# Optimization experiments

Hardware: AMD Instinct MI355X
Metric: run time of the kernel (lower is better)

The kernel has to match this reference:

```python
import jax, jax.numpy as jnp
import numpy as np

N_HEAD = 16    # config.n_head
T_STEPS = 3    # config.T: PC energy-minimization steps
LR = 0.01      # config.local_learning_rate


def _causal_attention(x, Wq, Wk, Wv):
    # x: [B, S, E] latent activity; generative model f(x) = causal MHA(x)
    B, S, E = x.shape
    D = E // N_HEAD
    def split(h):  # [B,S,E] -> [B,H,S,D]
        return h.reshape(B, S, N_HEAD, D).transpose(0, 2, 1, 3)
    q = split(x @ Wq.T)
    k = split(x @ Wk.T)
    v = split(x @ Wv.T)
    scores = jnp.einsum('bhqd,bhkd->bhqk', q, k) / jnp.sqrt(jnp.asarray(D, x.dtype))
    mask = jnp.tril(jnp.ones((S, S), dtype=bool))
    scores = jnp.where(mask, scores, jnp.asarray(-1e30, x.dtype))
    att = jax.nn.softmax(scores, axis=-1)
    out = jnp.einsum('bhqk,bhkd->bhqd', att, v)
    return out.transpose(0, 2, 1, 3).reshape(B, S, E)


def _pc_infer(target, f):
    # PCLayer: T steps of gradient descent on E(x) = 0.5 * ||target - f(x)||^2
    # x_init = 'zeros'; returns the inferred latent x (PCLayer.get_x).
    x = jnp.zeros_like(target)
    energy = lambda z: 0.5 * jnp.sum((target - f(z)) ** 2)
    g = jax.grad(energy)
    for _ in range(T_STEPS):  # fixed small T: unrolled
        x = x - LR * g(x)
    return x


def setup_inputs() -> dict:
    key = jax.random.key(0)
    ks = jax.random.split(key, 5)
    B, S, E = 2, 1024, 1024
    fc1_x = jax.random.normal(ks[0], (B, S, E), dtype=jnp.float32)
    init = lambda k: 0.02 * jax.random.normal(k, (E, E), dtype=jnp.float32)
    return {
        'fc1_x': fc1_x,
        'Wq': init(ks[1]),
        'Wk': init(ks[2]),
        'Wv': init(ks[3]),
        'Wo': init(ks[4]),
    }


def reference(fc1_x, Wq, Wk, Wv, Wo):
    # Stage 1 (pc_output): infer pre-output latent att_score s.t. output-proj
    # Wo @ att_score ~ fc1_x  (generative model f1(x) = x @ Wo^T, bias=False).
    att_score = _pc_infer(fc1_x, lambda z: z @ Wo.T)
    # Stage 2 (pc_qkv): infer latent x_qkv s.t. causal MHA(x_qkv) ~ att_score.
    x_qkv = _pc_infer(att_score, lambda z: _causal_attention(z, Wq, Wk, Wv))
    return x_qkv
```

## Files before the change

kernel.cpp:

```cpp
#include <hip/hip_runtime.h>
#include <hip/hip_bf16.h>
#include <math.h>

#define S_LEN 1024
#define E_DIM 1024
#define NH 16
#define HD 64
#define M_ROWS 2048
#define BH_CNT 32

static constexpr float LR_C = 0.01f;
static constexpr float SC_C = 0.125f;
static constexpr float C2_C = 0.125f * 1.44269504f;

typedef unsigned short ushort_t;
typedef __attribute__((ext_vector_type(8))) __bf16 bf16x8;
typedef __attribute__((ext_vector_type(4))) float f32x4;

static __device__ inline ushort_t f2bu(float f) {
  __hip_bfloat16 h = __float2bfloat16(f);
  return *(ushort_t*)&h;
}
static __device__ inline bf16x8 ldg8(const ushort_t* p) { return *(const bf16x8*)p; }

static __device__ inline void async_cp16(const ushort_t* g, __bf16* lds_wave_base) {
  __builtin_amdgcn_global_load_lds((const __attribute__((address_space(1))) void*)g,
                                   (__attribute__((address_space(3))) void*)lds_wave_base,
                                   16, 0, 0);
}

static __device__ inline void stage_tile(const ushort_t* src, size_t src_stride,
                                         ushort_t* lds, int lane, int wave) {
  int rl = lane >> 3;
  int c = ((lane & 7) - rl) & 7;
  #pragma unroll
  for (int t = 0; t < 2; t++) {
    int s = wave * 2 + t;
    async_cp16(src + (size_t)(s * 8 + rl) * src_stride + c * 8,
               (__bf16*)(lds + s * 512));
  }
}
static __device__ inline const bf16x8* tile_at(const ushort_t* lds, int r, int cchunk) {
  return (const bf16x8*)(lds + r * 64 + (((cchunk + r) & 7) * 8));
}

__global__ __launch_bounds__(256) void prep_w(const float* __restrict__ W,
                                              ushort_t* __restrict__ Wb,
                                              ushort_t* __restrict__ WTb) {
  __shared__ float ts[64][65];
  int bx = blockIdx.x * 64, by = blockIdx.y * 64;
  int t = threadIdx.x;
  int rr = t >> 6, cc = t & 63;
  #pragma unroll
  for (int p = 0; p < 16; p++) {
    int r = p * 4 + rr;
    float v = W[(size_t)(by + r) * E_DIM + bx + cc];
    ts[r][cc] = v;
    Wb[(size_t)(by + r) * E_DIM + bx + cc] = f2bu(v);
  }
  __syncthreads();
  #pragma unroll
  for (int p = 0; p < 16; p++) {
    int r = p * 4 + rr;
    WTb[(size_t)(bx + r) * E_DIM + by + cc] = f2bu(ts[cc][r]);
  }
}

__global__ __launch_bounds__(256) void k_cast(const float* __restrict__ in,
                                              ushort_t* __restrict__ out, int n4) {
  int i = blockIdx.x * 256 + threadIdx.x;
  if (i < n4) {
    float4 v = ((const float4*)in)[i];
    ushort_t p[4] = {f2bu(v.x), f2bu(v.y), f2bu(v.z), f2bu(v.w)};
    *(uint2*)(out + (size_t)i * 4) = *(uint2*)p;
  }
}

__global__ __launch_bounds__(256) void k_formN(const float* __restrict__ Mf,
                                               const float* __restrict__ M2f,
                                               ushort_t* __restrict__ Nb) {
  int idx = blockIdx.x * 256 + threadIdx.x;
  int i = idx >> 10, j = idx & 1023;
  float v = -3.f * LR_C * LR_C * Mf[idx] + LR_C * LR_C * LR_C * M2f[idx];
  if (i == j) v += 3.f * LR_C;
  Nb[idx] = f2bu(v);
}

__global__ __launch_bounds__(256) void k_scan1(const float* __restrict__ Xs,
                                               float* __restrict__ Sf,
                                               float* __restrict__ tot) {
  int e = blockIdx.x * 256 + threadIdx.x;
  int b = blockIdx.y;
  int z = blockIdx.z;
  float acc = 0.f;
  for (int i = z * 64 + 63; i >= z * 64; i--) {
    size_t idx = ((size_t)b * S_LEN + i) * E_DIM + e;
    acc = fmaf(Xs[idx], 1.0f / (float)(i + 1), acc);
    Sf[idx] = acc;
  }
  tot[((size_t)b * 16 + z) * E_DIM + e] = acc;
}

__global__ __launch_bounds__(256) void k_scan2(const float* __restrict__ Sf,
                                               const float* __restrict__ tot,
                                               ushort_t* __restrict__ Sb) {
  int e = blockIdx.x * 256 + threadIdx.x;
  int b = blockIdx.y;
  int z = blockIdx.z;
  float off = 0.f;
  for (int c = z + 1; c < 16; c++) off += tot[((size_t)b * 16 + c) * E_DIM + e];
  for (int i = z * 64; i < z * 64 + 64; i++) {
    size_t idx = ((size_t)b * S_LEN + i) * E_DIM + e;
    Sb[idx] = f2bu(Sf[idx] + off);
  }
}

template <int MODE, int NSEG>
__global__ __launch_bounds__(256) void gemm_mf(
    const ushort_t* __restrict__ A0, const ushort_t* __restrict__ A1, const ushort_t* __restrict__ A2,
    const ushort_t* __restrict__ B0, const ushort_t* __restrict__ B1, const ushort_t* __restrict__ B2,
    float* __restrict__ Cf,
    ushort_t* __restrict__ Cb0,
    float alpha) {
  const int K = 1024;
  __shared__ __bf16 As0[64][32];
  __shared__ __bf16 As1[64][32];
  __shared__ __bf16 Bs0[64][32];
  __shared__ __bf16 Bs1[64][32];
  int tid = threadIdx.x;
  int m0 = blockIdx.y * 64, n0 = blockIdx.x * 64;

  int lane = tid & 63, wave = tid >> 6;
  int wrow = wave >> 1, wcol = wave & 1;
  int fr = lane & 15, q = lane >> 4;

  int srow = wave * 16 + (lane >> 2);
  int scg = ((lane & 3) + (srow >> 1)) & 3;
  int scol = scg * 8;
  __bf16* ldsA0 = &As0[wave * 16][0];
  __bf16* ldsA1 = &As1[wave * 16][0];
  __bf16* ldsB0 = &Bs0[wave * 16][0];
  __bf16* ldsB1 = &Bs1[wave * 16][0];

  int rA0 = wrow * 32 + fr, rA1r = rA0 + 16;
  int rB0 = wcol * 32 + fr, rB1r = rB0 + 16;
  int cA0 = ((q - (rA0 >> 1)) & 3) * 8;
  int cA1 = ((q - (rA1r >> 1)) & 3) * 8;
  int cB0 = ((q - (rB0 >> 1)) & 3) * 8;
  int cB1 = ((q - (rB1r >> 1)) & 3) * 8;
  const bf16x8* pa0h0 = (const bf16x8*)&As0[rA0][cA0];
  const bf16x8* pa0h1 = (const bf16x8*)&As1[rA0][cA0];
  const bf16x8* pa1h0 = (const bf16x8*)&As0[rA1r][cA1];
  const bf16x8* pa1h1 = (const bf16x8*)&As1[rA1r][cA1];
  const bf16x8* pb0h0 = (const bf16x8*)&Bs0[rB0][cB0];
  const bf16x8* pb0h1 = (const bf16x8*)&Bs1[rB0][cB0];
  const bf16x8* pb1h0 = (const bf16x8*)&Bs0[rB1r][cB1];
  const bf16x8* pb1h1 = (const bf16x8*)&Bs1[rB1r][cB1];

  f32x4 acc[2][2] = {};

  #pragma unroll 1
  for (int seg = 0; seg < NSEG; seg++) {
    const ushort_t* Aseg = (seg == 0) ? A0 : (seg == 1) ? A1 : A2;
    const ushort_t* Bseg = (seg == 0) ? B0 : (seg == 1) ? B1 : B2;
    const ushort_t* ga = Aseg + (size_t)(m0 + srow) * K + scol;
    const ushort_t* gb = Bseg + (size_t)(n0 + srow) * K + scol;
    #pragma unroll 1
    for (int k0 = 0; k0 < K; k0 += 64) {
      __syncthreads();
      async_cp16(ga + k0, ldsA0);
      async_cp16(ga + k0 + 32, ldsA1);
      async_cp16(gb + k0, ldsB0);
      async_cp16(gb + k0 + 32, ldsB1);
      __syncthreads();
      bf16x8 a00 = *pa0h0, a01 = *pa0h1, a10 = *pa1h0, a11 = *pa1h1;
      bf16x8 b00 = *pb0h0, b01 = *pb0h1, b10 = *pb1h0, b11 = *pb1h1;
      acc[0][0] = __builtin_amdgcn_mfma_f32_16x16x32_bf16(a00, b00, acc[0][0], 0, 0, 0);
      acc[0][1] = __builtin_amdgcn_mfma_f32_16x16x32_bf16(a00, b10, acc[0][1], 0, 0, 0);
      acc[1][0] = __builtin_amdgcn_mfma_f32_16x16x32_bf16(a10, b00, acc[1][0], 0, 0, 0);
      acc[1][1] = __builtin_amdgcn_mfma_f32_16x16x32_bf16(a10, b10, acc[1][1], 0, 0, 0);
      acc[0][0] = __builtin_amdgcn_mfma_f32_16x16x32_bf16(a01, b01, acc[0][0], 0, 0, 0);
      acc[0][1] = __builtin_amdgcn_mfma_f32_16x16x32_bf16(a01, b11, acc[0][1], 0, 0, 0);
      acc[1][0] = __builtin_amdgcn_mfma_f32_16x16x32_bf16(a11, b01, acc[1][0], 0, 0, 0);
      acc[1][1] = __builtin_amdgcn_mfma_f32_16x16x32_bf16(a11, b11, acc[1][1], 0, 0, 0);
    }
  }

  #pragma unroll
  for (int mi = 0; mi < 2; mi++)
    #pragma unroll
    for (int ni = 0; ni < 2; ni++) {
      int col = n0 + wcol * 32 + ni * 16 + fr;
      int row0 = m0 + wrow * 32 + mi * 16 + q * 4;
      #pragma unroll
      for (int r = 0; r < 4; r++) {
        size_t idx = (size_t)(row0 + r) * E_DIM + col;
        float v = acc[mi][ni][r];
        if (MODE == 3) {
          Cf[idx] = v;
        } else if (MODE == 4) {
          Cf[idx] = v;
          Cb0[idx] = f2bu(v);
        } else if (MODE == 6) {
          float nv = alpha * v;
          Cf[idx] = nv;
          Cb0[idx] = f2bu(nv);
        } else {
          Cb0[idx] = f2bu(v);
        }
      }
    }
}

__global__ __launch_bounds__(256) void gemm_qkv(
    const ushort_t* __restrict__ A,
    const ushort_t* __restrict__ B0, const ushort_t* __restrict__ B1, const ushort_t* __restrict__ B2,
    ushort_t* __restrict__ Cb0, ushort_t* __restrict__ Cb1, ushort_t* __restrict__ Cb2,
    ushort_t* __restrict__ Ct0, ushort_t* __restrict__ Ct1, ushort_t* __restrict__ Ct2) {
  const int K = 1024;
  __shared__ __bf16 As[2][64][32];
  __shared__ __bf16 Bs[3][2][64][32];
  int tid = threadIdx.x;
  int m0 = blockIdx.y * 64, n0 = blockIdx.x * 64;

  int lane = tid & 63, wave = tid >> 6;
  int wrow = wave >> 1, wcol = wave & 1;
  int fr = lane & 15, q = lane >> 4;

  int srow = wave * 16 + (lane >> 2);
  int scg = ((lane & 3) + (srow >> 1)) & 3;
  int scol = scg * 8;
  __bf16* ldsA0 = &As[0][wave * 16][0];
  __bf16* ldsA1 = &As[1][wave * 16][0];
  __bf16* ldsB00 = &Bs[0][0][wave * 16][0];
  __bf16* ldsB01 = &Bs[0][1][wave * 16][0];
  __bf16* ldsB10 = &Bs[1][0][wave * 16][0];
  __bf16* ldsB11 = &Bs[1][1][wave * 16][0];
  __bf16* ldsB20 = &Bs[2][0][wave * 16][0];
  __bf16* ldsB21 = &Bs[2][1][wave * 16][0];

  int rA0 = wrow * 32 + fr, rA1r = rA0 + 16;
  int rB0 = wcol * 32 + fr, rB1r = rB0 + 16;
  int cA0 = ((q - (rA0 >> 1)) & 3) * 8;
  int cA1 = ((q - (rA1r >> 1)) & 3) * 8;
  int cB0 = ((q - (rB0 >> 1)) & 3) * 8;
  int cB1 = ((q - (rB1r >> 1)) & 3) * 8;
  const bf16x8* pa0h0 = (const bf16x8*)&As[0][rA0][cA0];
  const bf16x8* pa0h1 = (const bf16x8*)&As[1][rA0][cA0];
  const bf16x8* pa1h0 = (const bf16x8*)&As[0][rA1r][cA1];
  const bf16x8* pa1h1 = (const bf16x8*)&As[1][rA1r][cA1];

  f32x4 acc[3][2][2] = {};

  const ushort_t* ga = A + (size_t)(m0 + srow) * K + scol;
  const ushort_t* gb0 = B0 + (size_t)(n0 + srow) * K + scol;
  const ushort_t* gb1 = B1 + (size_t)(n0 + srow) * K + scol;
  const ushort_t* gb2 = B2 + (size_t)(n0 + srow) * K + scol;

  #pragma unroll 1
  for (int k0 = 0; k0 < K; k0 += 64) {
    __syncthreads();
    async_cp16(ga + k0, ldsA0);
    async_cp16(ga + k0 + 32, ldsA1);
    async_cp16(gb0 + k0, ldsB00);
    async_cp16(gb0 + k0 + 32, ldsB01);
    async_cp16(gb1 + k0, ldsB10);
    async_cp16(gb1 + k0 + 32, ldsB11);
    async_cp16(gb2 + k0, ldsB20);
    async_cp16(gb2 + k0 + 32, ldsB21);
    __syncthreads();
    bf16x8 a00 = *pa0h0, a01 = *pa0h1, a10 = *pa1h0, a11 = *pa1h1;
    #pragma unroll
    for (int z = 0; z < 3; z++) {
      bf16x8 b00 = *(const bf16x8*)&Bs[z][0][rB0][cB0];
      bf16x8 b01 = *(const bf16x8*)&Bs[z][1][rB0][cB0];
      bf16x8 b10 = *(const bf16x8*)&Bs[z][0][rB1r][cB1];
      bf16x8 b11 = *(const bf16x8*)&Bs[z][1][rB1r][cB1];
      acc[z][0][0] = __builtin_amdgcn_mfma_f32_16x16x32_bf16(a00, b00, acc[z][0][0], 0, 0, 0);
      acc[z][0][1] = __builtin_amdgcn_mfma_f32_16x16x32_bf16(a00, b10, acc[z][0][1], 0, 0, 0);
      acc[z][1][0] = __builtin_amdgcn_mfma_f32_16x16x32_bf16(a10, b00, acc[z][1][0], 0, 0, 0);
      acc[z][1][1] = __builtin_amdgcn_mfma_f32_16x16x32_bf16(a10, b10, acc[z][1][1], 0, 0, 0);
      acc[z][0][0] = __builtin_amdgcn_mfma_f32_16x16x32_bf16(a01, b01, acc[z][0][0], 0, 0, 0);
      acc[z][0][1] = __builtin_amdgcn_mfma_f32_16x16x32_bf16(a01, b11, acc[z][0][1], 0, 0, 0);
      acc[z][1][0] = __builtin_amdgcn_mfma_f32_16x16x32_bf16(a11, b01, acc[z][1][0], 0, 0, 0);
      acc[z][1][1] = __builtin_amdgcn_mfma_f32_16x16x32_bf16(a11, b11, acc[z][1][1], 0, 0, 0);
    }
  }

  #pragma unroll
  for (int z = 0; z < 3; z++) {
    ushort_t* Cbz = (z == 0) ? Cb0 : (z == 1) ? Cb1 : Cb2;
    ushort_t* Ctz = (z == 0) ? Ct0 : (z == 1) ? Ct1 : Ct2;
    float tsc = (z == 2) ? 1.0f : SC_C;
    #pragma unroll
    for (int mi = 0; mi < 2; mi++)
      #pragma unroll
      for (int ni = 0; ni < 2; ni++) {
        int col = n0 + wcol * 32 + ni * 16 + fr;
        int row0 = m0 + wrow * 32 + mi * 16 + q * 4;
        ushort_t pk[4];
        #pragma unroll
        for (int r = 0; r < 4; r++) {
          size_t idx = (size_t)(row0 + r) * E_DIM + col;
          float v = acc[z][mi][ni][r];
          Cbz[idx] = f2bu(v);
          pk[r] = f2bu(v * tsc);
        }
        int hh = col >> 6, dd = col & 63;
        int bb = row0 >> 10, ss = row0 & 1023;
        *(uint2*)(Ctz + ((size_t)((bb * NH + hh) * HD + dd)) * S_LEN + ss) = *(uint2*)pk;
      }
  }
}

__global__ __launch_bounds__(256) void gemm_acc(
    const ushort_t* __restrict__ A0, const ushort_t* __restrict__ A1, const ushort_t* __restrict__ A2,
    const ushort_t* __restrict__ B0, const ushort_t* __restrict__ B1, const ushort_t* __restrict__ B2,
    float* __restrict__ Cf, ushort_t* __restrict__ Cb, float alpha) {
  const int K = 1024;
  __shared__ __bf16 As[3][2][64][32];
  __shared__ __bf16 Bs[3][2][64][32];
  int tid = threadIdx.x;
  int m0 = blockIdx.y * 64, n0 = blockIdx.x * 64;

  int lane = tid & 63, wave = tid >> 6;
  int wrow = wave >> 1, wcol = wave & 1;
  int fr = lane & 15, q = lane >> 4;

  int srow = wave * 16 + (lane >> 2);
  int scg = ((lane & 3) + (srow >> 1)) & 3;
  int scol = scg * 8;

  int rA0 = wrow * 32 + fr, rA1r = rA0 + 16;
  int rB0 = wcol * 32 + fr, rB1r = rB0 + 16;
  int cA0 = ((q - (rA0 >> 1)) & 3) * 8;
  int cA1 = ((q - (rA1r >> 1)) & 3) * 8;
  int cB0 = ((q - (rB0 >> 1)) & 3) * 8;
  int cB1 = ((q - (rB1r >> 1)) & 3) * 8;

  f32x4 acc[3][2][2] = {};

  const ushort_t* ga0 = A0 + (size_t)(m0 + srow) * K + scol;
  const ushort_t* ga1 = A1 + (size_t)(m0 + srow) * K + scol;
  const ushort_t* ga2 = A2 + (size_t)(m0 + srow) * K + scol;
  const ushort_t* gb0 = B0 + (size_t)(n0 + srow) * K + scol;
  const ushort_t* gb1 = B1 + (size_t)(n0 + srow) * K + scol;
  const ushort_t* gb2 = B2 + (size_t)(n0 + srow) * K + scol;

  #pragma unroll 1
  for (int k0 = 0; k0 < K; k0 += 64) {
    __syncthreads();
    async_cp16(ga0 + k0,      &As[0][0][wave * 16][0]);
    async_cp16(ga0 + k0 + 32, &As[0][1][wave * 16][0]);
    async_cp16(ga1 + k0,      &As[1][0][wave * 16][0]);
    async_cp16(ga1 + k0 + 32, &As[1][1][wave * 16][0]);
    async_cp16(ga2 + k0,      &As[2][0][wave * 16][0]);
    async_cp16(ga2 + k0 + 32, &As[2][1][wave * 16][0]);
    async_cp16(gb0 + k0,      &Bs[0][0][wave * 16][0]);
    async_cp16(gb0 + k0 + 32, &Bs[0][1][wave * 16][0]);
    async_cp16(gb1 + k0,      &Bs[1][0][wave * 16][0]);
    async_cp16(gb1 + k0 + 32, &Bs[1][1][wave * 16][0]);
    async_cp16(gb2 + k0,      &Bs[2][0][wave * 16][0]);
    async_cp16(gb2 + k0 + 32, &Bs[2][1][wave * 16][0]);
    __syncthreads();
    #pragma unroll
    for (int z = 0; z < 3; z++) {
      bf16x8 a00 = *(const bf16x8*)&As[z][0][rA0][cA0];
      bf16x8 a01 = *(const bf16x8*)&As[z][1][rA0][cA0];
      bf16x8 a10 = *(const bf16x8*)&As[z][0][rA1r][cA1];
      bf16x8 a11 = *(const bf16x8*)&As[z][1][rA1r][cA1];
      bf16x8 b00 = *(const bf16x8*)&Bs[z][0][rB0][cB0];
      bf16x8 b01 = *(const bf16x8*)&Bs[z][1][rB0][cB0];
      bf16x8 b10 = *(const bf16x8*)&Bs[z][0][rB1r][cB1];
      bf16x8 b11 = *(const bf16x8*)&Bs[z][1][rB1r][cB1];
      acc[z][0][0] = __builtin_amdgcn_mfma_f32_16x16x32_bf16(a00, b00, acc[z][0][0], 0, 0, 0);
      acc[z][0][1] = __builtin_amdgcn_mfma_f32_16x16x32_bf16(a00, b10, acc[z][0][1], 0, 0, 0);
      acc[z][1][0] = __builtin_amdgcn_mfma_f32_16x16x32_bf16(a10, b00, acc[z][1][0], 0, 0, 0);
      acc[z][1][1] = __builtin_amdgcn_mfma_f32_16x16x32_bf16(a10, b10, acc[z][1][1], 0, 0, 0);
      acc[z][0][0] = __builtin_amdgcn_mfma_f32_16x16x32_bf16(a01, b01, acc[z][0][0], 0, 0, 0);
      acc[z][0][1] = __builtin_amdgcn_mfma_f32_16x16x32_bf16(a01, b11, acc[z][0][1], 0, 0, 0);
      acc[z][1][0] = __builtin_amdgcn_mfma_f32_16x16x32_bf16(a11, b01, acc[z][1][0], 0, 0, 0);
      acc[z][1][1] = __builtin_amdgcn_mfma_f32_16x16x32_bf16(a11, b11, acc[z][1][1], 0, 0, 0);
    }
  }

  #pragma unroll
  for (int mi = 0; mi < 2; mi++)
    #pragma unroll
    for (int ni = 0; ni < 2; ni++) {
      int col = n0 + wcol * 32 + ni * 16 + fr;
      int row0 = m0 + wrow * 32 + mi * 16 + q * 4;
      #pragma unroll
      for (int r = 0; r < 4; r++) {
        size_t idx = (size_t)(row0 + r) * E_DIM + col;
        float v = (acc[0][mi][ni][r] + acc[1][mi][ni][r]) + acc[2][mi][ni][r];
        float nv = Cf[idx] + alpha * v;
        Cf[idx] = nv;
        Cb[idx] = f2bu(nv);
      }
    }
}


__global__ __launch_bounds__(256) void fwd_fused(const ushort_t* __restrict__ Qg,
                                                 const ushort_t* __restrict__ Kg,
                                                 const ushort_t* __restrict__ Vt,
                                                 const float* __restrict__ Xs,
                                                 float* __restrict__ mbuf,
                                                 ushort_t* __restrict__ Gb,
                                                 ushort_t* __restrict__ Gt,
                                                 float* __restrict__ Dv) {
  int bh = blockIdx.x, y = blockIdx.y;
  int it = (y < 8) ? (15 - y) : (y - 8);
  int b = bh >> 4, h = bh & 15;
  int tid = threadIdx.x, lane = tid & 63, wv = tid >> 6;
  int fr = lane & 15, q = lane >> 4;
  int i0 = it * 64, band = wv * 16;
  __shared__ ushort_t Ks[4096];
  __shared__ ushort_t Vs[4096];
  __shared__ ushort_t Ps[64][72];

  const ushort_t* Kbase = Kg + (size_t)(b * S_LEN) * E_DIM + h * HD;
  const ushort_t* Vbase = Vt + (size_t)(bh * HD) * S_LEN;

  const ushort_t* Qrow = Qg + (size_t)(b * S_LEN + i0 + band + fr) * E_DIM + h * HD;
  bf16x8 aq0 = ldg8(Qrow + q * 8);
  bf16x8 aq1 = ldg8(Qrow + 32 + q * 8);

  float m[4], l[4];
  #pragma unroll
  for (int r = 0; r < 4; r++) { m[r] = -1e30f; l[r] = 0.f; }
  f32x4 oacc[4] = {};

  #pragma unroll 1
  for (int jt = 0; jt <= it; jt++) {
    int j0 = jt * 64;
    __syncthreads();
    stage_tile(Kbase + (size_t)j0 * E_DIM, E_DIM, Ks, lane, wv);
    stage_tile(Vbase + j0, S_LEN, Vs, lane, wv);
    __syncthreads();
    f32x4 sA[4];
    #pragma unroll
    for (int nc = 0; nc < 4; nc++) {
      bf16x8 bk0 = *tile_at(Ks, nc * 16 + fr, q);
      bf16x8 bk1 = *tile_at(Ks, nc * 16 + fr, q + 4);
      f32x4 z = {};
      z = __builtin_amdgcn_mfma_f32_16x16x32_bf16(aq0, bk0, z, 0, 0, 0);
      sA[nc] = __builtin_amdgcn_mfma_f32_16x16x32_bf16(aq1, bk1, z, 0, 0, 0);
    }
    float sv[4][4];
    #pragma unroll
    for (int nc = 0; nc < 4; nc++)
      #pragma unroll
      for (int r = 0; r < 4; r++) {
        int row = i0 + band + q * 4 + r;
        int col = j0 + nc * 16 + fr;
        sv[nc][r] = (col <= row) ? sA[nc][r] * C2_C : -1e30f;
      }
    #pragma unroll
    for (int r = 0; r < 4; r++) {
      float mx = fmaxf(fmaxf(sv[0][r], sv[1][r]), fmaxf(sv[2][r], sv[3][r]));
      #pragma unroll
      for (int off = 1; off < 16; off <<= 1) mx = fmaxf(mx, __shfl_xor(mx, off, 64));
      float mn = fmaxf(m[r], mx);
      float alpha = exp2f(m[r] - mn);
      float ps = 0.f;
      #pragma unroll
      for (int nc = 0; nc < 4; nc++) {
        float p = exp2f(sv[nc][r] - mn);
        Ps[band + q * 4 + r][nc * 16 + fr] = f2bu(p);
        ps += p;
      }
      l[r] = l[r] * alpha + ps;
      m[r] = mn;
      #pragma unroll
      for (int nc = 0; nc < 4; nc++) oacc[nc][r] *= alpha;
    }
    bf16x8 ap0 = *(const bf16x8*)&Ps[band + fr][q * 8];
    bf16x8 ap1 = *(const bf16x8*)&Ps[band + fr][32 + q * 8];
    #pragma unroll
    for (int nc = 0; nc < 4; nc++) {
      bf16x8 bv0 = *tile_at(Vs, nc * 16 + fr, q);
      bf16x8 bv1 = *tile_at(Vs, nc * 16 + fr, q + 4);
      oacc[nc] = __builtin_amdgcn_mfma_f32_16x16x32_bf16(ap0, bv0, oacc[nc], 0, 0, 0);
      oacc[nc] = __builtin_amdgcn_mfma_f32_16x16x32_bf16(ap1, bv1, oacc[nc], 0, 0, 0);
    }
  }
  #pragma unroll
  for (int r = 0; r < 4; r++) {
    #pragma unroll
    for (int off = 1; off < 16; off <<= 1) l[r] += __shfl_xor(l[r], off, 64);
  }
  float linv[4];
  #pragma unroll
  for (int r = 0; r < 4; r++) linv[r] = 1.0f / l[r];
  float dpart[4] = {};
  #pragma unroll
  for (int nc = 0; nc < 4; nc++) {
    ushort_t pg[4];
    #pragma unroll
    for (int r = 0; r < 4; r++) {
      int row = i0 + band + q * 4 + r;
      size_t gi = (size_t)(b * S_LEN + row) * E_DIM + h * HD + nc * 16 + fr;
      float o = oacc[nc][r] * linv[r];
      float g = o - Xs[gi];
      ushort_t bu = f2bu(g);
      Gb[gi] = bu;
      pg[r] = bu;
      dpart[r] += g * o;
    }
    int d = nc * 16 + fr;
    int s0 = i0 + band + q * 4;
    *(uint2*)(Gt + ((size_t)bh * HD + d) * S_LEN + s0) = *(uint2*)pg;
  }
  #pragma unroll
  for (int r = 0; r < 4; r++) {
    #pragma unroll
    for (int off = 1; off < 16; off <<= 1) dpart[r] += __shfl_xor(dpart[r], off, 64);
  }
  if (fr == 0) {
    #pragma unroll
    for (int r = 0; r < 4; r++) {
      size_t sid = (size_t)bh * S_LEN + i0 + band + q * 4 + r;
      mbuf[sid] = m[r] + log2f(l[r]);
      Dv[sid] = dpart[r];
    }
  }
}

__global__ __launch_bounds__(256) void bwd_fused(const ushort_t* __restrict__ Qg,
                                                 const ushort_t* __restrict__ Kg,
                                                 const ushort_t* __restrict__ Vg,
                                                 const ushort_t* __restrict__ Gg,
                                                 const ushort_t* __restrict__ Qt,
                                                 const ushort_t* __restrict__ Kt,
                                                 const ushort_t* __restrict__ Gt,
                                                 const float* __restrict__ mbuf,
                                                 const float* __restrict__ Dv,
                                                 ushort_t* __restrict__ GQ,
                                                 ushort_t* __restrict__ GK,
                                                 ushort_t* __restrict__ GV) {
  int bh = blockIdx.x, y = blockIdx.y;
  int b = bh >> 4, h = bh & 15;
  int tid = threadIdx.x, lane = tid & 63, wv = tid >> 6;
  int fr = lane & 15, q = lane >> 4;
  int band = wv * 16;
  __shared__ ushort_t tA[4][4096];
  __shared__ ushort_t tP[2][64][72];

  {
    ushort_t* Ks = tA[0];
    ushort_t* Vs = tA[1];
    ushort_t* Ts = tA[2];
    ushort_t (*dSs)[72] = tP[0];
    int it = y, i0 = it * 64;

    const ushort_t* KbaseA = Kg + (size_t)(b * S_LEN) * E_DIM + h * HD;
    const ushort_t* VbaseA = Vg + (size_t)(b * S_LEN) * E_DIM + h * HD;
    const ushort_t* TbaseA = Kt + (size_t)(bh * HD) * S_LEN;

    const ushort_t* Qrow = Qg + (size_t)(b * S_LEN + i0 + band + fr) * E_DIM + h * HD;
    const ushort_t* Grow = Gg + (size_t)(b * S_LEN + i0 + band + fr) * E_DIM + h * HD;
    bf16x8 aq0 = ldg8(Qrow + q * 8), aq1 = ldg8(Qrow + 32 + q * 8);
    bf16x8 ag0 = ldg8(Grow + q * 8), ag1 = ldg8(Grow + 32 + q * 8);

    float mrow[4], Dr[4];
    #pragma unroll
    for (int r = 0; r < 4; r++) {
      size_t sid = (size_t)bh * S_LEN + i0 + band + q * 4 + r;
      mrow[r] = mbuf[sid]; Dr[r] = Dv[sid];
    }
    f32x4 dqacc[4] = {};

    #pragma unroll 1
    for (int jt = 0; jt <= it; jt++) {
      int j0 = jt * 64;
      __syncthreads();
      stage_tile(KbaseA + (size_t)j0 * E_DIM, E_DIM, Ks, lane, wv);
      stage_tile(VbaseA + (size_t)j0 * E_DIM, E_DIM, Vs, lane, wv);
      stage_tile(TbaseA + j0, S_LEN, Ts, lane, wv);
      __syncthreads();
      f32x4 sA[4], dpA[4];
      #pragma unroll
      for (int nc = 0; nc < 4; nc++) {
        bf16x8 bk0 = *tile_at(Ks, nc * 16 + fr, q);
        bf16x8 bk1 = *tile_at(Ks, nc * 16 + fr, q + 4);
        bf16x8 bv0 = *tile_at(Vs, nc * 16 + fr, q);
        bf16x8 bv1 = *tile_at(Vs, nc * 16 + fr, q + 4);
        f32x4 z = {};
        z = __builtin_amdgcn_mfma_f32_16x16x32_bf16(aq0, bk0, z, 0, 0, 0);
        sA[nc] = __builtin_amdgcn_mfma_f32_16x16x32_bf16(aq1, bk1, z, 0, 0, 0);
        f32x4 z2 = {};
        z2 = __builtin_amdgcn_mfma_f32_16x16x32_bf16(ag0, bv0, z2, 0, 0, 0);
        dpA[nc] = __builtin_amdgcn_mfma_f32_16x16x32_bf16(ag1, bv1, z2, 0, 0, 0);
      }
      #pragma unroll
      for (int nc = 0; nc < 4; nc++)
        #pragma unroll
        for (int r = 0; r < 4; r++) {
          int row = i0 + band + q * 4 + r;
          int col = j0 + nc * 16 + fr;
          float ds = 0.f;
          if (col <= row) {
            float P = exp2f(fmaf(sA[nc][r], C2_C, -mrow[r]));
            ds = P * (dpA[nc][r] - Dr[r]);
          }
          dSs[band + q * 4 + r][nc * 16 + fr] = f2bu(ds);
        }
      bf16x8 ad0 = *(const bf16x8*)&dSs[band + fr][q * 8];
      bf16x8 ad1 = *(const bf16x8*)&dSs[band + fr][32 + q * 8];
      #pragma unroll
      for (int nc = 0; nc < 4; nc++) {
        bf16x8 bt0 = *tile_at(Ts, nc * 16 + fr, q);
        bf16x8 bt1 = *tile_at(Ts, nc * 16 + fr, q + 4);
        dqacc[nc] = __builtin_amdgcn_mfma_f32_16x16x32_bf16(ad0, bt0, dqacc[nc], 0, 0, 0);
        dqacc[nc] = __builtin_amdgcn_mfma_f32_16x16x32_bf16(ad1, bt1, dqacc[nc], 0, 0, 0);
      }
    }
    #pragma unroll
    for (int nc = 0; nc < 4; nc++)
      #pragma unroll
      for (int r = 0; r < 4; r++) {
        int row = i0 + band + q * 4 + r;
        size_t gi = (size_t)(b * S_LEN + row) * E_DIM + h * HD + nc * 16 + fr;
        GQ[gi] = f2bu(dqacc[nc][r]);
      }
  }

  {
    ushort_t* Qs  = tA[0];
    ushort_t* Gs  = tA[1];
    ushort_t* Qts = tA[2];
    ushort_t* Gts = tA[3];
    ushort_t (*PT)[72]  = tP[0];
    ushort_t (*dST)[72] = tP[1];
    int jt = y, j0 = jt * 64;

    const ushort_t* QbaseB = Qg + (size_t)(b * S_LEN) * E_DIM + h * HD;
    const ushort_t* GbaseB = Gg + (size_t)(b * S_LEN) * E_DIM + h * HD;
    const ushort_t* QtbaseB = Qt + (size_t)(bh * HD) * S_LEN;
    const ushort_t* GtbaseB = Gt + (size_t)(bh * HD) * S_LEN;

    const ushort_t* Krow = Kg + (size_t)(b * S_LEN + j0 + band + fr) * E_DIM + h * HD;
    const ushort_t* Vrow = Vg + (size_t)(b * S_LEN + j0 + band + fr) * E_DIM + h * HD;
    bf16x8 ak0 = ldg8(Krow + q * 8), ak1 = ldg8(Krow + 32 + q * 8);
    bf16x8 av0 = ldg8(Vrow + q * 8), av1 = ldg8(Vrow + 32 + q * 8);

    f32x4 dkacc[4] = {}, dvacc[4] = {};

    #pragma unroll 1
    for (int i_t = jt; i_t < 16; i_t++) {
      int i0 = i_t * 64;
      __syncthreads();
      stage_tile(QbaseB + (size_t)i0 * E_DIM, E_DIM, Qs, lane, wv);
      stage_tile(GbaseB + (size_t)i0 * E_DIM, E_DIM, Gs, lane, wv);
      stage_tile(QtbaseB + i0, S_LEN, Qts, lane, wv);
      stage_tile(GtbaseB + i0, S_LEN, Gts, lane, wv);
      __syncthreads();
      float mc[4], Dc[4];
      #pragma unroll
      for (int nc = 0; nc < 4; nc++) {
        size_t sid = (size_t)bh * S_LEN + i0 + nc * 16 + fr;
        mc[nc] = mbuf[sid]; Dc[nc] = Dv[sid];
      }
      f32x4 stA[4], dptA[4];
      #pragma unroll
      for (int nc = 0; nc < 4; nc++) {
        bf16x8 bq0 = *tile_at(Qs, nc * 16 + fr, q);
        bf16x8 bq1 = *tile_at(Qs, nc * 16 + fr, q + 4);
        bf16x8 bg0 = *tile_at(Gs, nc * 16 + fr, q);
        bf16x8 bg1 = *tile_at(Gs, nc * 16 + fr, q + 4);
        f32x4 z = {};
        z = __builtin_amdgcn_mfma_f32_16x16x32_bf16(ak0, bq0, z, 0, 0, 0);
        stA[nc] = __builtin_amdgcn_mfma_f32_16x16x32_bf16(ak1, bq1, z, 0, 0, 0);
        f32x4 z2 = {};
        z2 = __builtin_amdgcn_mfma_f32_16x16x32_bf16(av0, bg0, z2, 0, 0, 0);
        dptA[nc] = __builtin_amdgcn_mfma_f32_16x16x32_bf16(av1, bg1, z2, 0, 0, 0);
      }
      #pragma unroll
      for (int nc = 0; nc < 4; nc++)
        #pragma unroll
        for (int r = 0; r < 4; r++) {
          int jrow = j0 + band + q * 4 + r;
          int icol = i0 + nc * 16 + fr;
          float P = 0.f, ds = 0.f;
          if (icol >= jrow) {
            P = exp2f(fmaf(stA[nc][r], C2_C, -mc[nc]));
            ds = P * (dptA[nc][r] - Dc[nc]);
          }
          PT[band + q * 4 + r][nc * 16 + fr] = f2bu(P);
          dST[band + q * 4 + r][nc * 16 + fr] = f2bu(ds);
        }
      bf16x8 ap0 = *(const bf16x8*)&PT[band + fr][q * 8];
      bf16x8 ap1 = *(const bf16x8*)&PT[band + fr][32 + q * 8];
      bf16x8 ad0 = *(const bf16x8*)&dST[band + fr][q * 8];
      bf16x8 ad1 = *(const bf16x8*)&dST[band + fr][32 + q * 8];
      #pragma unroll
      for (int nc = 0; nc < 4; nc++) {
        bf16x8 bg0 = *tile_at(Gts, nc * 16 + fr, q);
        bf16x8 bg1 = *tile_at(Gts, nc * 16 + fr, q + 4);
        bf16x8 bq0 = *tile_at(Qts, nc * 16 + fr, q);
        bf16x8 bq1 = *tile_at(Qts, nc * 16 + fr, q + 4);
        dvacc[nc] = __builtin_amdgcn_mfma_f32_16x16x32_bf16(ap0, bg0, dvacc[nc], 0, 0, 0);
        dvacc[nc] = __builtin_amdgcn_mfma_f32_16x16x32_bf16(ap1, bg1, dvacc[nc], 0, 0, 0);
        dkacc[nc] = __builtin_amdgcn_mfma_f32_16x16x32_bf16(ad0, bq0, dkacc[nc], 0, 0, 0);
        dkacc[nc] = __builtin_amdgcn_mfma_f32_16x16x32_bf16(ad1, bq1, dkacc[nc], 0, 0, 0);
      }
    }
    #pragma unroll
    for (int nc = 0; nc < 4; nc++)
      #pragma unroll
      for (int r = 0; r < 4; r++) {
        int jrow = j0 + band + q * 4 + r;
        size_t gi = (size_t)(b * S_LEN + jrow) * E_DIM + h * HD + nc * 16 + fr;
        GK[gi] = f2bu(dkacc[nc][r]);
        GV[gi] = f2bu(dvacc[nc][r]);
      }
  }
}

extern "C" void kernel_launch(void* const* d_in, const int* in_sizes, int n_in,
                              void* d_out, int out_size, void* d_ws, size_t ws_size,
                              hipStream_t stream) {
  const float* T1 = (const float*)d_in[0];
  const float* Wq = (const float*)d_in[1];
  const float* Wk = (const float*)d_in[2];
  const float* Wv = (const float*)d_in[3];
  const float* Wo = (const float*)d_in[4];

  const size_t M2 = 2097152;
  const size_t M1 = 1048576;
  float* w = (float*)d_ws;
  float* Xs = w;
  float* mS = Xs + M2;
  float* DvS = mS + 65536;
  ushort_t* u = (ushort_t*)(DvS + 65536);
  ushort_t* W0 = u;          ushort_t* W1 = W0 + M1;  ushort_t* W2 = W1 + M1;
  ushort_t* W3 = W2 + M1;    ushort_t* W4 = W3 + M1;  ushort_t* W5 = W4 + M1;
  ushort_t* Qb = W5 + M1;    ushort_t* Kb = Qb + M2;  ushort_t* Vb = Kb + M2;
  ushort_t* Qt = Vb + M2;    ushort_t* Kt = Qt + M2;  ushort_t* Vt = Kt + M2;
  ushort_t* Gt = Vt + M2;
  ushort_t* Gb = Gt + M2;
  ushort_t* GQb = Gb + M2;   ushort_t* GKb = GQb + M2; ushort_t* GVb = GKb + M2;
  ushort_t* X2b = GVb + M2;
  float* X2 = (float*)d_out;

  float* Mf  = (float*)Qb;
  float* M2f = (float*)Kb;
  ushort_t* Mb  = Gt;
  ushort_t* Nb  = Vb;
  ushort_t* AtB = Qt;
  ushort_t* T1b = Kt;

  float* Sf  = (float*)GQb;
  float* tot = mS;
  ushort_t* Sb = GVb;

  dim3 pgrid(16, 16);
  dim3 sgrid(16, 16);
  dim3 ggrid(16, 32);
  dim3 agrid(BH_CNT, 16);

  k_cast<<<(M2 / 4 + 255) / 256, 256, 0, stream>>>(T1, T1b, (int)(M2 / 4));
  prep_w<<<pgrid, 256, 0, stream>>>(Wo, W0, W1);
  gemm_mf<4, 1><<<sgrid, 256, 0, stream>>>(W1, nullptr, nullptr, W1, nullptr, nullptr,
                                           Mf, Mb, 0.f);
  gemm_mf<3, 1><<<sgrid, 256, 0, stream>>>(Mb, nullptr, nullptr, Mb, nullptr, nullptr,
                                           M2f, nullptr, 0.f);
  k_formN<<<(M1 + 255) / 256, 256, 0, stream>>>(Mf, M2f, Nb);
  gemm_mf<5, 1><<<sgrid, 256, 0, stream>>>(Nb, nullptr, nullptr, W0, nullptr, nullptr,
                                           nullptr, AtB, 0.f);
  prep_w<<<pgrid, 256, 0, stream>>>(Wq, W0, W3);
  prep_w<<<pgrid, 256, 0, stream>>>(Wk, W1, W4);
  prep_w<<<pgrid, 256, 0, stream>>>(Wv, W2, W5);
  gemm_mf<3, 1><<<ggrid, 256, 0, stream>>>(T1b, nullptr, nullptr, AtB, nullptr, nullptr,
                                           Xs, nullptr, 0.f);

  k_scan1<<<dim3(E_DIM / 256, 2, 16), 256, 0, stream>>>(Xs, Sf, tot);
  k_scan2<<<dim3(E_DIM / 256, 2, 16), 256, 0, stream>>>(Sf, tot, Sb);
  gemm_mf<6, 1><<<ggrid, 256, 0, stream>>>(Sb, nullptr, nullptr, W5, nullptr, nullptr,
                                           X2, X2b, LR_C);

  for (int t = 1; t < 3; t++) {
    gemm_qkv<<<ggrid, 256, 0, stream>>>(X2b, W0, W1, W2,
                                        Qb, Kb, Vb, Qt, Kt, Vt);
    fwd_fused<<<agrid, 256, 0, stream>>>(Qb, Kb, Vt, Xs, mS, Gb, Gt, DvS);
    bwd_fused<<<agrid, 256, 0, stream>>>(Qb, Kb, Vb, Gb, Qt, Kt, Gt, mS, DvS,
                                         GQb, GKb, GVb);
    gemm_acc<<<ggrid, 256, 0, stream>>>(GQb, GKb, GVb, W3, W4, W5,
                                        X2, X2b, -LR_C);
  }
}
```

Measured before the change: 429.4 us.

## Double-buffer LDS tiles in forward and backward attention kernels

The K/V and Q/G/transposed tiles are now staged into alternating LDS buffers, so the next tile is loaded while the current one is used. This removes one block barrier per loop iteration. In bwd_fused, the P and dS scratch tiles share a single buffer that is written and read one after the other within each wave. The aim is to hide global-load latency behind MFMA work, at the cost of more LDS per block in the backward kernel (about 73KB instead of about 50KB), which may lower the number of resident blocks per CU.

```diff
diff --git a/kernel.cpp b/kernel.cpp
--- a/kernel.cpp
+++ b/kernel.cpp
@@ -416,8 +416,8 @@
   int tid = threadIdx.x, lane = tid & 63, wv = tid >> 6;
   int fr = lane & 15, q = lane >> 4;
   int i0 = it * 64, band = wv * 16;
-  __shared__ ushort_t Ks[4096];
-  __shared__ ushort_t Vs[4096];
+  __shared__ ushort_t Ksb[2][4096];
+  __shared__ ushort_t Vsb[2][4096];
   __shared__ ushort_t Ps[64][72];
 
   const ushort_t* Kbase = Kg + (size_t)(b * S_LEN) * E_DIM + h * HD;
@@ -432,13 +432,21 @@
   for (int r = 0; r < 4; r++) { m[r] = -1e30f; l[r] = 0.f; }
   f32x4 oacc[4] = {};
 
+  stage_tile(Kbase, E_DIM, Ksb[0], lane, wv);
+  stage_tile(Vbase, S_LEN, Vsb[0], lane, wv);
+
   #pragma unroll 1
   for (int jt = 0; jt <= it; jt++) {
     int j0 = jt * 64;
+    int cur = jt & 1;
     __syncthreads();
-    stage_tile(Kbase + (size_t)j0 * E_DIM, E_DIM, Ks, lane, wv);
-    stage_tile(Vbase + j0, S_LEN, Vs, lane, wv);
-    __syncthreads();
+    if (jt < it) {
+      int j0n = j0 + 64;
+      stage_tile(Kbase + (size_t)j0n * E_DIM, E_DIM, Ksb[cur ^ 1], lane, wv);
+      stage_tile(Vbase + j0n, S_LEN, Vsb[cur ^ 1], lane, wv);
+    }
+    const ushort_t* Ks = Ksb[cur];
+    const ushort_t* Vs = Vsb[cur];
     f32x4 sA[4];
     #pragma unroll
     for (int nc = 0; nc < 4; nc++) {
@@ -545,14 +553,10 @@
   int tid = threadIdx.x, lane = tid & 63, wv = tid >> 6;
   int fr = lane & 15, q = lane >> 4;
   int band = wv * 16;
-  __shared__ ushort_t tA[4][4096];
-  __shared__ ushort_t tP[2][64][72];
+  __shared__ ushort_t tA[8][4096];
+  __shared__ ushort_t tP[64][72];
 
   {
-    ushort_t* Ks = tA[0];
-    ushort_t* Vs = tA[1];
-    ushort_t* Ts = tA[2];
-    ushort_t (*dSs)[72] = tP[0];
     int it = y, i0 = it * 64;
 
     const ushort_t* KbaseA = Kg + (size_t)(b * S_LEN) * E_DIM + h * HD;
@@ -572,14 +576,25 @@
     }
     f32x4 dqacc[4] = {};
 
+    stage_tile(KbaseA, E_DIM, tA[0], lane, wv);
+    stage_tile(VbaseA, E_DIM, tA[1], lane, wv);
+    stage_tile(TbaseA, S_LEN, tA[2], lane, wv);
+
     #pragma unroll 1
     for (int jt = 0; jt <= it; jt++) {
+      int cur = (jt & 1) * 3;
+      __syncthreads();
+      if (jt < it) {
+        int j0n = (jt + 1) * 64;
+        int nxt = 3 - cur;
+        stage_tile(KbaseA + (size_t)j0n * E_DIM, E_DIM, tA[nxt], lane, wv);
+        stage_tile(VbaseA + (size_t)j0n * E_DIM, E_DIM, tA[nxt + 1], lane, wv);
+        stage_tile(TbaseA + j0n, S_LEN, tA[nxt + 2], lane, wv);
+      }
+      const ushort_t* Ks = tA[cur];
+      const ushort_t* Vs = tA[cur + 1];
+      const ushort_t* Ts = tA[cur + 2];
       int j0 = jt * 64;
-      __syncthreads();
-      stage_tile(KbaseA + (size_t)j0 * E_DIM, E_DIM, Ks, lane, wv);
-      stage_tile(VbaseA + (size_t)j0 * E_DIM, E_DIM, Vs, lane, wv);
-      stage_tile(TbaseA + j0, S_LEN, Ts, lane, wv);
-      __syncthreads();
       f32x4 sA[4], dpA[4];
       #pragma unroll
       for (int nc = 0; nc < 4; nc++) {
@@ -605,10 +620,10 @@
             float P = exp2f(fmaf(sA[nc][r], C2_C, -mrow[r]));
             ds = P * (dpA[nc][r] - Dr[r]);
           }
-          dSs[band + q * 4 + r][nc * 16 + fr] = f2bu(ds);
+          tP[band + q * 4 + r][nc * 16 + fr] = f2bu(ds);
         }
-      bf16x8 ad0 = *(const bf16x8*)&dSs[band + fr][q * 8];
-      bf16x8 ad1 = *(const bf16x8*)&dSs[band + fr][32 + q * 8];
+      bf16x8 ad0 = *(const bf16x8*)&tP[band + fr][q * 8];
+      bf16x8 ad1 = *(const bf16x8*)&tP[band + fr][32 + q * 8];
       #pragma unroll
       for (int nc = 0; nc < 4; nc++) {
         bf16x8 bt0 = *tile_at(Ts, nc * 16 + fr, q);
@@ -617,6 +632,7 @@
         dqacc[nc] = __builtin_amdgcn_mfma_f32_16x16x32_bf16(ad1, bt1, dqacc[nc], 0, 0, 0);
       }
     }
+    __syncthreads();
     #pragma unroll
     for (int nc = 0; nc < 4; nc++)
       #pragma unroll
@@ -628,12 +644,6 @@
   }
 
   {
-    ushort_t* Qs  = tA[0];
-    ushort_t* Gs  = tA[1];
-    ushort_t* Qts = tA[2];
-    ushort_t* Gts = tA[3];
-    ushort_t (*PT)[72]  = tP[0];
-    ushort_t (*dST)[72] = tP[1];
     int jt = y, j0 = jt * 64;
 
     const ushort_t* QbaseB = Qg + (size_t)(b * S_LEN) * E_DIM + h * HD;
@@ -648,15 +658,28 @@
 
     f32x4 dkacc[4] = {}, dvacc[4] = {};
 
+    stage_tile(QbaseB + (size_t)j0 * E_DIM, E_DIM, tA[0], lane, wv);
+    stage_tile(GbaseB + (size_t)j0 * E_DIM, E_DIM, tA[1], lane, wv);
+    stage_tile(QtbaseB + j0, S_LEN, tA[2], lane, wv);
+    stage_tile(GtbaseB + j0, S_LEN, tA[3], lane, wv);
+
     #pragma unroll 1
     for (int i_t = jt; i_t < 16; i_t++) {
+      int cur = ((i_t - jt) & 1) * 4;
+      __syncthreads();
+      if (i_t < 15) {
+        int i0n = (i_t + 1) * 64;
+        int nxt = 4 - cur;
+        stage_tile(QbaseB + (size_t)i0n * E_DIM, E_DIM, tA[nxt], lane, wv);
+        stage_tile(GbaseB + (size_t)i0n * E_DIM, E_DIM, tA[nxt + 1], lane, wv);
+        stage_tile(QtbaseB + i0n, S_LEN, tA[nxt + 2], lane, wv);
+        stage_tile(GtbaseB + i0n, S_LEN, tA[nxt + 3], lane, wv);
+      }
+      const ushort_t* Qs  = tA[cur];
+      const ushort_t* Gs  = tA[cur + 1];
+      const ushort_t* Qts = tA[cur + 2];
+      const ushort_t* Gts = tA[cur + 3];
       int i0 = i_t * 64;
-      __syncthreads();
-      stage_tile(QbaseB + (size_t)i0 * E_DIM, E_DIM, Qs, lane, wv);
-      stage_tile(GbaseB + (size_t)i0 * E_DIM, E_DIM, Gs, lane, wv);
-      stage_tile(QtbaseB + i0, S_LEN, Qts, lane, wv);
-      stage_tile(GtbaseB + i0, S_LEN, Gts, lane, wv);
-      __syncthreads();
       float mc[4], Dc[4];
       #pragma unroll
       for (int nc = 0; nc < 4; nc++) {
@@ -677,6 +700,7 @@
         z2 = __builtin_amdgcn_mfma_f32_16x16x32_bf16(av0, bg0, z2, 0, 0, 0);
         dptA[nc] = __builtin_amdgcn_mfma_f32_16x16x32_bf16(av1, bg1, z2, 0, 0, 0);
       }
+      ushort_t dsp[4][4];
       #pragma unroll
       for (int nc = 0; nc < 4; nc++)
         #pragma unroll
@@ -688,21 +712,29 @@
             P = exp2f(fmaf(stA[nc][r], C2_C, -mc[nc]));
             ds = P * (dptA[nc][r] - Dc[nc]);
           }
-          PT[band + q * 4 + r][nc * 16 + fr] = f2bu(P);
-          dST[band + q * 4 + r][nc * 16 + fr] = f2bu(ds);
+          dsp[nc][r] = f2bu(ds);
+          tP[band + q * 4 + r][nc * 16 + fr] = f2bu(P);
         }
-      bf16x8 ap0 = *(const bf16x8*)&PT[band + fr][q * 8];
-      bf16x8 ap1 = *(const bf16x8*)&PT[band + fr][32 + q * 8];
-      bf16x8 ad0 = *(const bf16x8*)&dST[band + fr][q * 8];
-      bf16x8 ad1 = *(const bf16x8*)&dST[band + fr][32 + q * 8];
+      bf16x8 ap0 = *(const bf16x8*)&tP[band + fr][q * 8];
+      bf16x8 ap1 = *(const bf16x8*)&tP[band + fr][32 + q * 8];
       #pragma unroll
       for (int nc = 0; nc < 4; nc++) {
         bf16x8 bg0 = *tile_at(Gts, nc * 16 + fr, q);
         bf16x8 bg1 = *tile_at(Gts, nc * 16 + fr, q + 4);
+        dvacc[nc] = __builtin_amdgcn_mfma_f32_16x16x32_bf16(ap0, bg0, dvacc[nc], 0, 0, 0);
+        dvacc[nc] = __builtin_amdgcn_mfma_f32_16x16x32_bf16(ap1, bg1, dvacc[nc], 0, 0, 0);
+      }
+      #pragma unroll
+      for (int nc = 0; nc < 4; nc++)
+        #pragma unroll
+        for (int r = 0; r < 4; r++)
+          tP[band + q * 4 + r][nc * 16 + fr] = dsp[nc][r];
+      bf16x8 ad0 = *(const bf16x8*)&tP[band + fr][q * 8];
+      bf16x8 ad1 = *(const bf16x8*)&tP[band + fr][32 + q * 8];
+      #pragma unroll
+      for (int nc = 0; nc < 4; nc++) {
         bf16x8 bq0 = *tile_at(Qts, nc * 16 + fr, q);
         bf16x8 bq1 = *tile_at(Qts, nc * 16 + fr, q + 4);
-        dvacc[nc] = __builtin_amdgcn_mfma_f32_16x16x32_bf16(ap0, bg0, dvacc[nc], 0, 0, 0);
-        dvacc[nc] = __builtin_amdgcn_mfma_f32_16x16x32_bf16(ap1, bg1, dvacc[nc], 0, 0, 0);
         dkacc[nc] = __builtin_amdgcn_mfma_f32_16x16x32_bf16(ad0, bq0, dkacc[nc], 0, 0, 0);
         dkacc[nc] = __builtin_amdgcn_mfma_f32_16x16x32_bf16(ad1, bq1, dkacc[nc], 0, 0, 0);
       }
```

Measured after the change: 426.7 us. No clear change (-0.6%).
